# Optimization experiments

Hardware: AMD Instinct MI355X
Metric: run time of the kernel (lower is better)

Reference implementation:

```python
import jax, jax.numpy as jnp
import numpy as np

# Graph/batch constants (compressed-edge representation of graph.adjmat)
B, N, E, D = 64, 1024, 1_048_576, 128        # graphs, nodes/graph, edges, new_edge_dim
EDGE_DIM, MSSG_DIM, GLOB_DIM, CNDT_DIM = 64, 32, 8, 8
HIDDEN, N_HEADS = 256, 4
HEAD_DIM = D // N_HEADS                        # 32
ATTN_IN = MSSG_DIM + EDGE_DIM + GLOB_DIM + CNDT_DIM  # 112
NUM_SEG = B * N


def setup_inputs() -> dict:
    key = jax.random.key(0)
    ks = jax.random.split(key, 11)
    new_edges = jax.random.normal(ks[0], (E, D), dtype=jnp.float32)
    edges = jax.random.normal(ks[1], (E, EDGE_DIM), dtype=jnp.float32)
    pooled_mssgs = jax.random.normal(ks[2], (E, MSSG_DIM), dtype=jnp.float32)
    globs = jax.random.normal(ks[3], (B, GLOB_DIM), dtype=jnp.float32)
    cndts = jax.random.normal(ks[4], (B, CNDT_DIM), dtype=jnp.float32)
    W1 = jax.random.normal(ks[5], (ATTN_IN, HIDDEN), dtype=jnp.float32) * (1.0 / np.sqrt(ATTN_IN))
    b1 = jnp.zeros((HIDDEN,), dtype=jnp.float32)
    W2 = jax.random.normal(ks[6], (HIDDEN, N_HEADS), dtype=jnp.float32) * (1.0 / np.sqrt(HIDDEN))
    b2 = jnp.zeros((N_HEADS,), dtype=jnp.float32)
    batch_idx = jnp.sort(jax.random.randint(ks[7], (E,), 0, B, dtype=jnp.int32))
    recv_idx = jax.random.randint(ks[8], (E,), 0, N, dtype=jnp.int32)
    return dict(new_edges=new_edges, edges=edges, pooled_mssgs=pooled_mssgs,
                globs=globs, cndts=cndts, W1=W1, b1=b1, W2=W2, b2=b2,
                batch_idx=batch_idx, recv_idx=recv_idx)


def reference(new_edges, edges, pooled_mssgs, globs, cndts, W1, b1, W2, b2,
              batch_idx, recv_idx):
    # ctxt_from_mask: broadcast per-graph globs/cndts to each compressed edge  [E, g+c]
    ctxt = jnp.concatenate([globs[batch_idx], cndts[batch_idx]], axis=-1)
    # smart_cat([pooled_mssgs, graph.edges]) + ctxt concat inside DenseNetwork
    x = jnp.concatenate([pooled_mssgs, edges, ctxt], axis=-1)      # [E, 112]
    h = jax.nn.leaky_relu(x @ W1 + b1, 0.1)                        # [E, 256]
    logits = h @ W2 + b2                                           # [E, n_heads]

    # segment id = (graph, receiver) slot; adjmat nonzeros -> compressed edges
    seg = batch_idx * N + recv_idx                                 # [E]

    # aggr_via_sparse(..., reduction='softmax', dim=1): masked segment softmax per head
    m = jax.ops.segment_max(logits, seg, num_segments=NUM_SEG)     # [B*N, H]
    ex = jnp.exp(logits - m[seg])
    denom = jax.ops.segment_sum(ex, seg, num_segments=NUM_SEG)
    attn = ex / denom[seg]                                         # [E, H]

    # unsqueeze(-1).expand(-1,-1,head_dim).flatten(1) == repeat each head head_dim times
    w = jnp.repeat(attn, HEAD_DIM, axis=1)                         # [E, D]

    # aggr_via_sparse(..., 'sum', dim=1) then decompress onto dense [B, N, D]
    pooled = jax.ops.segment_sum(new_edges * w, seg, num_segments=NUM_SEG)
    return pooled.reshape(B, N, D)
```

## Files before the change

kernel.cpp:

```cpp
#include <hip/hip_runtime.h>
#include <hip/hip_bf16.h>
#include <cstdint>
#include <cstddef>

#define E_TOT   1048576
#define BGR     64
#define NN      1024
#define DD      128
#define HID     256
#define NH      4
#define NSEG    65536
#define KDIM    96
#define NKCH    12
#define BM      64
#define NTILES  (E_TOT/BM)
#define GRIDM   512
#define TPB     (NTILES/GRIDM)

typedef __attribute__((ext_vector_type(8))) short s16x8;
typedef __attribute__((ext_vector_type(4))) float f32x4;

static __device__ __forceinline__ unsigned short f2bf_rn(float f) {
    unsigned u = __float_as_uint(f);
    unsigned r = u + 0x7FFF + ((u >> 16) & 1);
    return (unsigned short)(r >> 16);
}

__global__ __launch_bounds__(256)
void k_misc(const float* __restrict__ W1, const float* __restrict__ b1,
            const float* __restrict__ globs, const float* __restrict__ cndts,
            const int* __restrict__ batch_idx, const int* __restrict__ recv_idx,
            short* __restrict__ Wg, float* __restrict__ ctxtc,
            int* __restrict__ counts)
{
    const int bid = blockIdx.x;
    const int tid = threadIdx.x;
    if (bid < 4096) {
        int e = bid * 256 + tid;
        atomicAdd(&counts[batch_idx[e] * NN + recv_idx[e]], 1);
    } else if (bid < 4096 + 96) {
        int idx = (bid - 4096) * 256 + tid;
        int kchunk = idx >> 11;
        int n      = (idx >> 3) & 255;
        int j      = idx & 7;
        int k      = kchunk * 8 + j;
        Wg[idx] = (short)f2bf_rn(W1[k * 256 + n]);
    } else {
        int b = bid - 4192, j = tid;
        float s = b1[j];
        #pragma unroll
        for (int g = 0; g < 8; ++g) s = fmaf(globs[b * 8 + g], W1[(96 + g) * 256 + j], s);
        #pragma unroll
        for (int c = 0; c < 8; ++c) s = fmaf(cndts[b * 8 + c], W1[(104 + c) * 256 + j], s);
        ctxtc[b * 256 + j] = s;
    }
}

__global__ __launch_bounds__(256)
void k_scan1(const int* __restrict__ counts, int* __restrict__ tmp_excl,
             int* __restrict__ blocksums)
{
    __shared__ int sh[256];
    const int t = threadIdx.x;
    const int gid = blockIdx.x * 256 + t;
    int c = counts[gid];
    sh[t] = c;
    __syncthreads();
    int v = c;
    for (int off = 1; off < 256; off <<= 1) {
        int u = (t >= off) ? sh[t - off] : 0;
        __syncthreads();
        v += u; sh[t] = v;
        __syncthreads();
    }
    tmp_excl[gid] = v - c;
    if (t == 255) blocksums[blockIdx.x] = v;
}

__global__ __launch_bounds__(256)
void k_scan3(const int* __restrict__ tmp_excl, const int* __restrict__ blocksums,
             int* __restrict__ offsets, int* __restrict__ cursor)
{
    __shared__ int swv[4];
    const int t = threadIdx.x;
    const int bid = blockIdx.x;
    int v = (t < bid) ? blocksums[t] : 0;
    #pragma unroll
    for (int off = 1; off < 64; off <<= 1) v += __shfl_xor(v, off);
    if ((t & 63) == 0) swv[t >> 6] = v;
    __syncthreads();
    const int base = swv[0] + swv[1] + swv[2] + swv[3];
    const int gid = bid * 256 + t;
    int o = tmp_excl[gid] + base;
    offsets[gid] = o;
    cursor[gid]  = o;
}

__global__ __launch_bounds__(512, 4)
void k_mlp_mfma(const float* __restrict__ pooled, const float* __restrict__ edges,
                const short* __restrict__ Wg,     const float* __restrict__ ctxtc,
                const float* __restrict__ W2,
                const int* __restrict__ batch_idx, const int* __restrict__ recv_idx,
                float* __restrict__ ex_out, float* __restrict__ denom,
                int* __restrict__ cursor, int* __restrict__ elist)
{
    __shared__ short Wl[NKCH * 256 * 8];
    __shared__ short Xl[NKCH * BM * 8];
    __shared__ float sW2[256 * 4];
    __shared__ float plog[4][BM][4];

    const int tid  = threadIdx.x;
    const int lane = tid & 63;
    const int wid  = tid >> 6;
    const int la   = lane & 15;
    const int g    = lane >> 4;
    const int es   = wid & 1;
    const int hq   = wid >> 1;

    {
        const float4* src = reinterpret_cast<const float4*>(Wg);
        float4* dst = reinterpret_cast<float4*>(Wl);
        #pragma unroll
        for (int i = 0; i < 6; ++i) dst[i * 512 + tid] = src[i * 512 + tid];
        if (tid < 256)
            *reinterpret_cast<float4*>(&sW2[tid * 4]) =
                reinterpret_cast<const float4*>(W2)[tid];
    }

    const int u0 = tid;
    const int u1 = tid + 512;
    const int e_u0 = u0 / 12, k_u0 = u0 - e_u0 * 12;
    const int e_u1 = u1 / 12, k_u1 = u1 - e_u1 * 12;

    {
        const int e0 = blockIdx.x * TPB * BM;
        {
            const int eg = e0 + e_u0;
            const float* p = (k_u0 < 4) ? (pooled + (size_t)eg * 32 + k_u0 * 8)
                                        : (edges + (size_t)eg * 64 + (k_u0 - 4) * 8);
            float4 v0 = reinterpret_cast<const float4*>(p)[0];
            float4 v1 = reinterpret_cast<const float4*>(p)[1];
            float vals[8] = {v0.x,v0.y,v0.z,v0.w,v1.x,v1.y,v1.z,v1.w};
            s16x8 hv;
            #pragma unroll
            for (int i = 0; i < 8; ++i) hv[i] = (short)f2bf_rn(vals[i]);
            *reinterpret_cast<s16x8*>(&Xl[(k_u0 * BM + e_u0) * 8]) = hv;
        }
        if (tid < 256) {
            const int eg = e0 + e_u1;
            const float* p = (k_u1 < 4) ? (pooled + (size_t)eg * 32 + k_u1 * 8)
                                        : (edges + (size_t)eg * 64 + (k_u1 - 4) * 8);
            float4 v0 = reinterpret_cast<const float4*>(p)[0];
            float4 v1 = reinterpret_cast<const float4*>(p)[1];
            float vals[8] = {v0.x,v0.y,v0.z,v0.w,v1.x,v1.y,v1.z,v1.w};
            s16x8 hv;
            #pragma unroll
            for (int i = 0; i < 8; ++i) hv[i] = (short)f2bf_rn(vals[i]);
            *reinterpret_cast<s16x8*>(&Xl[(k_u1 * BM + e_u1) * 8]) = hv;
        }
    }
    __syncthreads();

    for (int t = 0; t < TPB; ++t) {
        const int e0 = (blockIdx.x * TPB + t) * BM;
        const bool has_next = (t + 1 < TPB);

        float4 sa0, sa1, sb0, sb1;
        if (has_next) {
            const int en = e0 + BM;
            {
                const int eg = en + e_u0;
                const float* p = (k_u0 < 4) ? (pooled + (size_t)eg * 32 + k_u0 * 8)
                                            : (edges + (size_t)eg * 64 + (k_u0 - 4) * 8);
                sa0 = reinterpret_cast<const float4*>(p)[0];
                sa1 = reinterpret_cast<const float4*>(p)[1];
            }
            if (tid < 256) {
                const int eg = en + e_u1;
                const float* p = (k_u1 < 4) ? (pooled + (size_t)eg * 32 + k_u1 * 8)
                                            : (edges + (size_t)eg * 64 + (k_u1 - 4) * 8);
                sb0 = reinterpret_cast<const float4*>(p)[0];
                sb1 = reinterpret_cast<const float4*>(p)[1];
            }
        }

        f32x4 acc[4][2];
        #pragma unroll
        for (int i = 0; i < 4; ++i) {
            acc[i][0] = (f32x4){0.f, 0.f, 0.f, 0.f};
            acc[i][1] = (f32x4){0.f, 0.f, 0.f, 0.f};
        }
        #pragma unroll
        for (int ks = 0; ks < 3; ++ks) {
            const int kb = ks * 4 + g;
            const s16x8 xf0 = *reinterpret_cast<const s16x8*>(
                &Xl[(kb * BM + es * 32 + la) * 8]);
            const s16x8 xf1 = *reinterpret_cast<const s16x8*>(
                &Xl[(kb * BM + es * 32 + 16 + la) * 8]);
            const short* wrow = &Wl[(kb * 256 + hq * 64 + la) * 8];
            #pragma unroll
            for (int hf = 0; hf < 4; ++hf) {
                s16x8 wf = *reinterpret_cast<const s16x8*>(wrow + hf * 128);
                acc[hf][0] = __builtin_amdgcn_mfma_f32_16x16x32_bf16(wf, xf0, acc[hf][0], 0, 0, 0);
                acc[hf][1] = __builtin_amdgcn_mfma_f32_16x16x32_bf16(wf, xf1, acc[hf][1], 0, 0, 0);
            }
        }

        {
            const int ea = e0 + es * 32 + la;
            const int eb = ea + 16;
            const int ba = batch_idx[ea];
            const int bb = batch_idx[eb];
            const float* cxa_base = &ctxtc[(size_t)ba * 256 + hq * 64 + g * 4];
            const float* cxb_base = &ctxtc[(size_t)bb * 256 + hq * 64 + g * 4];
            float pa0 = 0.f, pa1 = 0.f, pa2 = 0.f, pa3 = 0.f;
            float pb0 = 0.f, pb1 = 0.f, pb2 = 0.f, pb3 = 0.f;
            #pragma unroll
            for (int hf = 0; hf < 4; ++hf) {
                const float4 cxa = *reinterpret_cast<const float4*>(cxa_base + hf * 16);
                const float4 cxb = *reinterpret_cast<const float4*>(cxb_base + hf * 16);
                const float cxaa[4] = {cxa.x, cxa.y, cxa.z, cxa.w};
                const float cxba[4] = {cxb.x, cxb.y, cxb.z, cxb.w};
                #pragma unroll
                for (int r = 0; r < 4; ++r) {
                    const int j = hq * 64 + hf * 16 + g * 4 + r;
                    const float4 w2v = *reinterpret_cast<const float4*>(&sW2[j * 4]);
                    float sa = acc[hf][0][r] + cxaa[r];
                    float ha = fmaxf(sa, 0.1f * sa);
                    float sb = acc[hf][1][r] + cxba[r];
                    float hb = fmaxf(sb, 0.1f * sb);
                    pa0 = fmaf(ha, w2v.x, pa0); pb0 = fmaf(hb, w2v.x, pb0);
                    pa1 = fmaf(ha, w2v.y, pa1); pb1 = fmaf(hb, w2v.y, pb1);
                    pa2 = fmaf(ha, w2v.z, pa2); pb2 = fmaf(hb, w2v.z, pb2);
                    pa3 = fmaf(ha, w2v.w, pa3); pb3 = fmaf(hb, w2v.w, pb3);
                }
            }
            pa0 += __shfl_xor(pa0, 16); pa0 += __shfl_xor(pa0, 32);
            pa1 += __shfl_xor(pa1, 16); pa1 += __shfl_xor(pa1, 32);
            pa2 += __shfl_xor(pa2, 16); pa2 += __shfl_xor(pa2, 32);
            pa3 += __shfl_xor(pa3, 16); pa3 += __shfl_xor(pa3, 32);
            pb0 += __shfl_xor(pb0, 16); pb0 += __shfl_xor(pb0, 32);
            pb1 += __shfl_xor(pb1, 16); pb1 += __shfl_xor(pb1, 32);
            pb2 += __shfl_xor(pb2, 16); pb2 += __shfl_xor(pb2, 32);
            pb3 += __shfl_xor(pb3, 16); pb3 += __shfl_xor(pb3, 32);
            float pla = (g == 0) ? pa0 : (g == 1) ? pa1 : (g == 2) ? pa2 : pa3;
            float plb = (g == 0) ? pb0 : (g == 1) ? pb1 : (g == 2) ? pb2 : pb3;
            plog[hq][es * 32 + la][g]      = pla;
            plog[hq][es * 32 + 16 + la][g] = plb;
        }
        __syncthreads();

        if (has_next) {
            {
                float vals[8] = {sa0.x,sa0.y,sa0.z,sa0.w,sa1.x,sa1.y,sa1.z,sa1.w};
                s16x8 hv;
                #pragma unroll
                for (int i = 0; i < 8; ++i) hv[i] = (short)f2bf_rn(vals[i]);
                *reinterpret_cast<s16x8*>(&Xl[(k_u0 * BM + e_u0) * 8]) = hv;
            }
            if (tid < 256) {
                float vals[8] = {sb0.x,sb0.y,sb0.z,sb0.w,sb1.x,sb1.y,sb1.z,sb1.w};
                s16x8 hv;
                #pragma unroll
                for (int i = 0; i < 8; ++i) hv[i] = (short)f2bf_rn(vals[i]);
                *reinterpret_cast<s16x8*>(&Xl[(k_u1 * BM + e_u1) * 8]) = hv;
            }
        }

        if (tid < 256) {
            const int e = tid >> 2;
            const int h = tid & 3;
            const int eg = e0 + e;
            float lg = plog[0][e][h] + plog[1][e][h] + plog[2][e][h] + plog[3][e][h];
            float exv = __expf(lg);
            ex_out[(size_t)eg * 4 + h] = exv;
            const int seg = batch_idx[eg] * NN + recv_idx[eg];
            atomicAdd(&denom[seg * 4 + h], exv);
            if (h == 0) {
                int pos = atomicAdd(&cursor[seg], 1);
                elist[pos] = eg;
            }
        }
        __syncthreads();
    }
}

__global__ __launch_bounds__(256)
void k_gather(const float* __restrict__ new_edges, const float* __restrict__ ex,
              const float* __restrict__ denom, const int* __restrict__ offsets,
              const int* __restrict__ counts, const int* __restrict__ elist,
              float* __restrict__ out)
{
    const int gid  = blockIdx.x * 256 + threadIdx.x;
    const int seg  = gid >> 6;
    const int lane = threadIdx.x & 63;
    if (seg >= NSEG) return;

    const int start = offsets[seg];
    const int cnt   = counts[seg];
    const int h     = lane >> 4;
    const int doff  = lane * 2;

    float a0 = 0.f, a1 = 0.f;
    int i = 0;
    for (; i + 4 <= cnt; i += 4) {
        const int el0 = elist[start + i + 0];
        const int el1 = elist[start + i + 1];
        const int el2 = elist[start + i + 2];
        const int el3 = elist[start + i + 3];
        const float w0 = ex[(size_t)el0 * 4 + h];
        const float w1 = ex[(size_t)el1 * 4 + h];
        const float w2 = ex[(size_t)el2 * 4 + h];
        const float w3 = ex[(size_t)el3 * 4 + h];
        const float2 n0 = *reinterpret_cast<const float2*>(new_edges + (size_t)el0 * DD + doff);
        const float2 n1 = *reinterpret_cast<const float2*>(new_edges + (size_t)el1 * DD + doff);
        const float2 n2 = *reinterpret_cast<const float2*>(new_edges + (size_t)el2 * DD + doff);
        const float2 n3 = *reinterpret_cast<const float2*>(new_edges + (size_t)el3 * DD + doff);
        a0 = fmaf(n0.x, w0, a0); a1 = fmaf(n0.y, w0, a1);
        a0 = fmaf(n1.x, w1, a0); a1 = fmaf(n1.y, w1, a1);
        a0 = fmaf(n2.x, w2, a0); a1 = fmaf(n2.y, w2, a1);
        a0 = fmaf(n3.x, w3, a0); a1 = fmaf(n3.y, w3, a1);
    }
    for (; i < cnt; ++i) {
        const int el = elist[start + i];
        const float w = ex[(size_t)el * 4 + h];
        const float2 n = *reinterpret_cast<const float2*>(new_edges + (size_t)el * DD + doff);
        a0 = fmaf(n.x, w, a0); a1 = fmaf(n.y, w, a1);
    }
    const float scale = (cnt > 0) ? 1.0f / denom[seg * 4 + h] : 0.0f;
    float2 r; r.x = a0 * scale; r.y = a1 * scale;
    *reinterpret_cast<float2*>(out + (size_t)seg * DD + doff) = r;
}

extern "C" void kernel_launch(void* const* d_in, const int* in_sizes, int n_in,
                              void* d_out, int out_size, void* d_ws, size_t ws_size,
                              hipStream_t stream)
{
    const float* new_edges = (const float*)d_in[0];
    const float* edges     = (const float*)d_in[1];
    const float* pooled    = (const float*)d_in[2];
    const float* globs     = (const float*)d_in[3];
    const float* cndts     = (const float*)d_in[4];
    const float* W1        = (const float*)d_in[5];
    const float* b1        = (const float*)d_in[6];
    const float* W2        = (const float*)d_in[7];
    const int*   batch_idx = (const int*)d_in[9];
    const int*   recv_idx  = (const int*)d_in[10];
    float* out = (float*)d_out;

    char* ws = (char*)d_ws;
    float* ex       = (float*)(ws);
    float* denom    = (float*)(ws + (size_t)16 * 1024 * 1024);
    char*  base17   = ws + (size_t)17 * 1024 * 1024;
    int*   counts   = (int*)(base17);
    int*   offs     = (int*)(base17 + 1 * 262144);
    int*   cursor   = (int*)(base17 + 2 * 262144);
    int*   tmp_excl = (int*)(base17 + 3 * 262144);
    int*   bsums    = (int*)(base17 + 4 * 262144);
    int*   elist    = (int*)(ws + (size_t)18 * 1024 * 1024);
    short* Wg       = (short*)(ws + (size_t)22 * 1024 * 1024);
    float* ctxtc    = (float*)(ws + (size_t)22 * 1024 * 1024 + 65536);

    hipMemsetAsync(denom, 0,
                   (size_t)NSEG * NH * sizeof(float) + (size_t)NSEG * sizeof(int),
                   stream);

    k_misc<<<4096 + 96 + 64, 256, 0, stream>>>(W1, b1, globs, cndts,
                                               batch_idx, recv_idx,
                                               Wg, ctxtc, counts);
    k_scan1<<<NSEG / 256, 256, 0, stream>>>(counts, tmp_excl, bsums);
    k_scan3<<<NSEG / 256, 256, 0, stream>>>(tmp_excl, bsums, offs, cursor);

    k_mlp_mfma<<<GRIDM, 512, 0, stream>>>(pooled, edges, Wg, ctxtc, W2,
                                          batch_idx, recv_idx, ex, denom,
                                          cursor, elist);

    k_gather<<<(NSEG * 64) / 256, 256, 0, stream>>>(new_edges, ex, denom,
                                                    offs, counts, elist, out);
}
```

Baseline: 325.6 us.

## Double-buffer X tile and logits to drop a per-tile barrier

The MLP kernel now keeps two X tiles and two logit scratch buffers, which removes one of the two __syncthreads per tile. The next tile's conversion can then overlap the exp/atomic epilogue of the current tile. W2 is read directly from global memory (cached) instead of being staged in LDS, and the edge-count histogram kernel uses int4 loads so each thread handles four edges. The cost is more LDS per block, which may lower occupancy, plus repeated global reads of W2 in the inner epilogue.

```diff
diff --git a/kernel.cpp b/kernel.cpp
--- a/kernel.cpp
+++ b/kernel.cpp
@@ -35,18 +35,23 @@
 {
     const int bid = blockIdx.x;
     const int tid = threadIdx.x;
-    if (bid < 4096) {
-        int e = bid * 256 + tid;
-        atomicAdd(&counts[batch_idx[e] * NN + recv_idx[e]], 1);
-    } else if (bid < 4096 + 96) {
-        int idx = (bid - 4096) * 256 + tid;
+    if (bid < 1024) {
+        int e4 = (bid * 256 + tid) * 4;
+        const int4 b4 = *reinterpret_cast<const int4*>(batch_idx + e4);
+        const int4 r4 = *reinterpret_cast<const int4*>(recv_idx + e4);
+        atomicAdd(&counts[b4.x * NN + r4.x], 1);
+        atomicAdd(&counts[b4.y * NN + r4.y], 1);
+        atomicAdd(&counts[b4.z * NN + r4.z], 1);
+        atomicAdd(&counts[b4.w * NN + r4.w], 1);
+    } else if (bid < 1024 + 96) {
+        int idx = (bid - 1024) * 256 + tid;
         int kchunk = idx >> 11;
         int n      = (idx >> 3) & 255;
         int j      = idx & 7;
         int k      = kchunk * 8 + j;
         Wg[idx] = (short)f2bf_rn(W1[k * 256 + n]);
     } else {
-        int b = bid - 4192, j = tid;
+        int b = bid - 1120, j = tid;
         float s = b1[j];
         #pragma unroll
         for (int g = 0; g < 8; ++g) s = fmaf(globs[b * 8 + g], W1[(96 + g) * 256 + j], s);
@@ -105,9 +110,8 @@
                 int* __restrict__ cursor, int* __restrict__ elist)
 {
     __shared__ short Wl[NKCH * 256 * 8];
-    __shared__ short Xl[NKCH * BM * 8];
-    __shared__ float sW2[256 * 4];
-    __shared__ float plog[4][BM][4];
+    __shared__ short Xl[2][NKCH * BM * 8];
+    __shared__ float plog[2][4][BM][4];
 
     const int tid  = threadIdx.x;
     const int lane = tid & 63;
@@ -122,9 +126,6 @@
         float4* dst = reinterpret_cast<float4*>(Wl);
         #pragma unroll
         for (int i = 0; i < 6; ++i) dst[i * 512 + tid] = src[i * 512 + tid];
-        if (tid < 256)
-            *reinterpret_cast<float4*>(&sW2[tid * 4]) =
-                reinterpret_cast<const float4*>(W2)[tid];
     }
 
     const int u0 = tid;
@@ -144,7 +145,7 @@
             s16x8 hv;
             #pragma unroll
             for (int i = 0; i < 8; ++i) hv[i] = (short)f2bf_rn(vals[i]);
-            *reinterpret_cast<s16x8*>(&Xl[(k_u0 * BM + e_u0) * 8]) = hv;
+            *reinterpret_cast<s16x8*>(&Xl[0][(k_u0 * BM + e_u0) * 8]) = hv;
         }
         if (tid < 256) {
             const int eg = e0 + e_u1;
@@ -156,12 +157,14 @@
             s16x8 hv;
             #pragma unroll
             for (int i = 0; i < 8; ++i) hv[i] = (short)f2bf_rn(vals[i]);
-            *reinterpret_cast<s16x8*>(&Xl[(k_u1 * BM + e_u1) * 8]) = hv;
+            *reinterpret_cast<s16x8*>(&Xl[0][(k_u1 * BM + e_u1) * 8]) = hv;
         }
     }
     __syncthreads();
 
     for (int t = 0; t < TPB; ++t) {
+        const int cur = t & 1;
+        const int nxt = cur ^ 1;
         const int e0 = (blockIdx.x * TPB + t) * BM;
         const bool has_next = (t + 1 < TPB);
 
@@ -194,9 +197,9 @@
         for (int ks = 0; ks < 3; ++ks) {
             const int kb = ks * 4 + g;
             const s16x8 xf0 = *reinterpret_cast<const s16x8*>(
-                &Xl[(kb * BM + es * 32 + la) * 8]);
+                &Xl[cur][(kb * BM + es * 32 + la) * 8]);
             const s16x8 xf1 = *reinterpret_cast<const s16x8*>(
-                &Xl[(kb * BM + es * 32 + 16 + la) * 8]);
+                &Xl[cur][(kb * BM + es * 32 + 16 + la) * 8]);
             const short* wrow = &Wl[(kb * 256 + hq * 64 + la) * 8];
             #pragma unroll
             for (int hf = 0; hf < 4; ++hf) {
@@ -224,7 +227,7 @@
                 #pragma unroll
                 for (int r = 0; r < 4; ++r) {
                     const int j = hq * 64 + hf * 16 + g * 4 + r;
-                    const float4 w2v = *reinterpret_cast<const float4*>(&sW2[j * 4]);
+                    const float4 w2v = *reinterpret_cast<const float4*>(&W2[j * 4]);
                     float sa = acc[hf][0][r] + cxaa[r];
                     float ha = fmaxf(sa, 0.1f * sa);
                     float sb = acc[hf][1][r] + cxba[r];
@@ -245,10 +248,9 @@
             pb3 += __shfl_xor(pb3, 16); pb3 += __shfl_xor(pb3, 32);
             float pla = (g == 0) ? pa0 : (g == 1) ? pa1 : (g == 2) ? pa2 : pa3;
             float plb = (g == 0) ? pb0 : (g == 1) ? pb1 : (g == 2) ? pb2 : pb3;
-            plog[hq][es * 32 + la][g]      = pla;
-            plog[hq][es * 32 + 16 + la][g] = plb;
-        }
-        __syncthreads();
+            plog[cur][hq][es * 32 + la][g]      = pla;
+            plog[cur][hq][es * 32 + 16 + la][g] = plb;
+        }
 
         if (has_next) {
             {
@@ -256,22 +258,25 @@
                 s16x8 hv;
                 #pragma unroll
                 for (int i = 0; i < 8; ++i) hv[i] = (short)f2bf_rn(vals[i]);
-                *reinterpret_cast<s16x8*>(&Xl[(k_u0 * BM + e_u0) * 8]) = hv;
+                *reinterpret_cast<s16x8*>(&Xl[nxt][(k_u0 * BM + e_u0) * 8]) = hv;
             }
             if (tid < 256) {
                 float vals[8] = {sb0.x,sb0.y,sb0.z,sb0.w,sb1.x,sb1.y,sb1.z,sb1.w};
                 s16x8 hv;
                 #pragma unroll
                 for (int i = 0; i < 8; ++i) hv[i] = (short)f2bf_rn(vals[i]);
-                *reinterpret_cast<s16x8*>(&Xl[(k_u1 * BM + e_u1) * 8]) = hv;
-            }
-        }
+                *reinterpret_cast<s16x8*>(&Xl[nxt][(k_u1 * BM + e_u1) * 8]) = hv;
+            }
+        }
+
+        __syncthreads();
 
         if (tid < 256) {
             const int e = tid >> 2;
             const int h = tid & 3;
             const int eg = e0 + e;
-            float lg = plog[0][e][h] + plog[1][e][h] + plog[2][e][h] + plog[3][e][h];
+            float lg = plog[cur][0][e][h] + plog[cur][1][e][h]
+                     + plog[cur][2][e][h] + plog[cur][3][e][h];
             float exv = __expf(lg);
             ex_out[(size_t)eg * 4 + h] = exv;
             const int seg = batch_idx[eg] * NN + recv_idx[eg];
@@ -281,7 +286,6 @@
                 elist[pos] = eg;
             }
         }
-        __syncthreads();
     }
 }
 
@@ -365,7 +369,7 @@
                    (size_t)NSEG * NH * sizeof(float) + (size_t)NSEG * sizeof(int),
                    stream);
 
-    k_misc<<<4096 + 96 + 64, 256, 0, stream>>>(W1, b1, globs, cndts,
+    k_misc<<<1024 + 96 + 64, 256, 0, stream>>>(W1, b1, globs, cndts,
                                                batch_idx, recv_idx,
                                                Wg, ctxtc, counts);
     k_scan1<<<NSEG / 256, 256, 0, stream>>>(counts, tmp_excl, bsums);
```

Result: slower. 542.7 us (+66.7%).
